# Optimization experiments

Hardware: AMD Instinct MI355X
Metric: run time of the kernel (lower is better)

Reference implementation:

```python
import jax, jax.numpy as jnp
import numpy as np

EMB = 1024
HEADS = 8
EXP = 4
EPS = 1e-5


def setup_inputs() -> dict:
    key = jax.random.key(0)
    ks = jax.random.split(key, 12)
    s = 0.02
    return {
        "x": jax.random.normal(ks[0], (4, 2048, EMB), dtype=jnp.float32),
        "wqkv_w": jax.random.normal(ks[1], (EMB, 3 * EMB), dtype=jnp.float32) * s,
        "wqkv_b": jnp.zeros((3 * EMB,), dtype=jnp.float32),
        "proj_w": jax.random.normal(ks[2], (EMB, EMB), dtype=jnp.float32) * s,
        "proj_b": jnp.zeros((EMB,), dtype=jnp.float32),
        "lin1_w": jax.random.normal(ks[3], (EMB, EXP * EMB), dtype=jnp.float32) * s,
        "lin1_b": jnp.zeros((EXP * EMB,), dtype=jnp.float32),
        "lin2_w": jax.random.normal(ks[4], (EXP * EMB, EMB), dtype=jnp.float32) * s,
        "lin2_b": jnp.zeros((EMB,), dtype=jnp.float32),
        "ln_g": jnp.ones((EMB,), dtype=jnp.float32),
        "ln_b": jnp.zeros((EMB,), dtype=jnp.float32),
    }


def _layernorm(x, g, b):
    mu = jnp.mean(x, axis=-1, keepdims=True)
    var = jnp.var(x, axis=-1, keepdims=True)
    return (x - mu) * jax.lax.rsqrt(var + EPS) * g + b


def reference(x, wqkv_w, wqkv_b, proj_w, proj_b, lin1_w, lin1_b, lin2_w, lin2_b, ln_g, ln_b):
    b, n, e = x.shape
    h = HEADS
    d = e // h
    # fused QKV; source splits '(h d w)' with w=3 innermost (interleaved)
    w = x @ wqkv_w + wqkv_b                      # [b, n, 3e]
    w = w.reshape(b, n, h, d, 3)
    w = jnp.transpose(w, (4, 0, 2, 1, 3))        # [3, b, h, n, d]
    q, k, v = w[0], w[1], w[2]
    scores = jnp.einsum('bhqd,bhkd->bhqk', q, k)  # unscaled logits (as in source)
    attn = jax.nn.softmax(scores, axis=-1) / jnp.sqrt(jnp.float32(e))
    o = jnp.einsum('bhqk,bhkd->bhqd', attn, v)
    o = jnp.transpose(o, (0, 2, 1, 3)).reshape(b, n, e)
    mha = o @ proj_w + proj_b
    x = _layernorm(x + mha, ln_g, ln_b)
    ff = (jax.nn.gelu(x @ lin1_w + lin1_b, approximate=False)) @ lin2_w + lin2_b
    return _layernorm(x + ff, ln_g, ln_b)
```

## Files before the change

kernel.cpp:

```cpp
#include <hip/hip_runtime.h>
#include <hip/hip_bf16.h>
#include <math.h>

#define B_DIM 4
#define SEQ   2048
#define EMB   1024
#define HEADS 8
#define DHEAD 128
#define M_TOK (B_DIM * SEQ)
#define FFDIM (4 * EMB)

typedef unsigned short u16;
typedef __attribute__((ext_vector_type(8))) short short8v;
typedef __attribute__((ext_vector_type(4))) float float4v;
typedef __attribute__((ext_vector_type(16))) float float16v;

__device__ __forceinline__ u16 f2b(float f) {
  union { float f; unsigned u; } a; a.f = f;
  unsigned u = a.u;
  u += 0x7fffu + ((u >> 16) & 1u);
  return (u16)(u >> 16);
}

__device__ __forceinline__ u16 f2b_hw(float f) {
  __hip_bfloat16 h = __float2bfloat16(f);
  return *(u16*)&h;
}

__device__ __forceinline__ void gload16(const void* g, void* l) {
  __builtin_amdgcn_global_load_lds(
      (const __attribute__((address_space(1))) unsigned int*)g,
      (__attribute__((address_space(3))) unsigned int*)l, 16, 0, 0);
}

__device__ __forceinline__ float gelu_inl(float v) {
  const float y = 0.7978845608028654f * (v + 0.044715f * v * v * v);
  const float e = __expf(2.0f * y);
  const float th = 1.0f - 2.0f / (e + 1.0f);
  return 0.5f * v * (1.0f + th);
}

__device__ __forceinline__ void tcvt_body(const float* __restrict__ W,
    u16* __restrict__ Wt, int K, int N, int bx, int by, int tx, int ty,
    float (*t)[33]) {
  const int n0 = bx * 32, k0 = by * 32;
  for (int j = ty; j < 32; j += 8)
    t[j][tx] = W[(size_t)(k0 + j) * N + n0 + tx];
  __syncthreads();
  for (int j = ty; j < 32; j += 8)
    Wt[(size_t)(n0 + j) * K + k0 + tx] = f2b(t[tx][j]);
}

__global__ __launch_bounds__(256) void k_prep(
    const float* __restrict__ x, const float* __restrict__ wqkv_w,
    const float* __restrict__ proj_w, const float* __restrict__ lin1_w,
    const float* __restrict__ lin2_w, u16* __restrict__ xb,
    u16* __restrict__ wqkv_t, u16* __restrict__ proj_t,
    u16* __restrict__ lin1_t, u16* __restrict__ lin2_t) {
  __shared__ float t[32][33];
  const int bid = blockIdx.x, tid = threadIdx.x;
  if (bid < 8192) {
    const int i = bid * 256 + tid;
    const float4 v = ((const float4*)x)[i];
    unsigned long long pk = (unsigned long long)f2b(v.x)
        | ((unsigned long long)f2b(v.y) << 16)
        | ((unsigned long long)f2b(v.z) << 32)
        | ((unsigned long long)f2b(v.w) << 48);
    ((unsigned long long*)xb)[i] = pk;
    return;
  }
  const int tx = tid & 31, ty = tid >> 5;
  if (bid < 11264)
    tcvt_body(wqkv_w, wqkv_t, 1024, 3072, (bid - 8192) % 96, (bid - 8192) / 96, tx, ty, t);
  else if (bid < 12288)
    tcvt_body(proj_w, proj_t, 1024, 1024, (bid - 11264) % 32, (bid - 11264) / 32, tx, ty, t);
  else if (bid < 16384)
    tcvt_body(lin1_w, lin1_t, 1024, 4096, (bid - 12288) % 128, (bid - 12288) / 128, tx, ty, t);
  else
    tcvt_body(lin2_w, lin2_t, 4096, 1024, (bid - 16384) % 32, (bid - 16384) / 32, tx, ty, t);
}

template <int EPI>
__global__ __launch_bounds__(256, 2) void k_gemm(
    const u16* __restrict__ A, const u16* __restrict__ Bt,
    const float* __restrict__ bias, const float* __restrict__ res,
    void* __restrict__ out0, int M, int N, int K) {
  __shared__ __align__(16) u16 lds[2][2][128][32];
  const int tid = threadIdx.x;
  const int l = tid & 63, w = tid >> 6;
  const int g = l >> 4, lm = l & 15;
  const int wm = w >> 1, wn = w & 1;

  const int NBX = N >> 7;
  const int nwg = NBX * (M >> 7);
  const int wg = blockIdx.x;
  const int swz = (wg & 7) * (nwg >> 3) + (wg >> 3);
  const int tn = swz % NBX, tm = swz / NBX;

  const size_t arow0 = (size_t)tm * 128;
  const size_t brow0 = (size_t)tn * 128;
  const int srow = l >> 2;
  const int scol = (l & 3) * 8;

  float4v acc[4][4];
  const float4v vzero = {0.f, 0.f, 0.f, 0.f};
#pragma unroll
  for (int i = 0; i < 4; ++i)
#pragma unroll
    for (int j = 0; j < 4; ++j) acc[i][j] = vzero;

  const int nt = K / 32;
  auto stage = [&](int t, int buf) {
    const int k0 = t * 32;
#pragma unroll
    for (int i = 0; i < 2; ++i) {
      const int r = w * 32 + i * 16 + srow;
      gload16(A + (arow0 + r) * (size_t)K + k0 + scol, &lds[buf][0][w * 32 + i * 16][0]);
      gload16(Bt + (brow0 + r) * (size_t)K + k0 + scol, &lds[buf][1][w * 32 + i * 16][0]);
    }
  };

  stage(0, 0);
  __syncthreads();
  for (int t = 0; t < nt; ++t) {
    const int buf = t & 1;
    if (t + 1 < nt) stage(t + 1, buf ^ 1);
    short8v af[4], bf[4];
#pragma unroll
    for (int mf = 0; mf < 4; ++mf)
      af[mf] = *(const short8v*)&lds[buf][0][wm * 64 + mf * 16 + lm][g * 8];
#pragma unroll
    for (int nf = 0; nf < 4; ++nf)
      bf[nf] = *(const short8v*)&lds[buf][1][wn * 64 + nf * 16 + lm][g * 8];
#pragma unroll
    for (int mf = 0; mf < 4; ++mf)
#pragma unroll
      for (int nf = 0; nf < 4; ++nf)
        acc[mf][nf] = __builtin_amdgcn_mfma_f32_16x16x32_bf16(af[mf], bf[nf], acc[mf][nf], 0, 0, 0);
    __syncthreads();
  }

#pragma unroll
  for (int mf = 0; mf < 4; ++mf)
#pragma unroll
    for (int nf = 0; nf < 4; ++nf)
#pragma unroll
      for (int r = 0; r < 4; ++r) {
        const int row = tm * 128 + wm * 64 + mf * 16 + 4 * g + r;
        const int col = tn * 128 + wn * 64 + nf * 16 + lm;
        float v = acc[mf][nf][r] + bias[col];
        if constexpr (EPI == 0) {
          const int hh = col / 384;
          const int rem = col - hh * 384;
          const int d = rem / 3;
          const int wv = rem - d * 3;
          const int btok = row >> 11, ntok = row & 2047;
          u16* dst = (u16*)out0 + (size_t)wv * ((size_t)M_TOK * EMB)
                   + (((size_t)(btok * HEADS + hh) * SEQ + ntok) * DHEAD + d);
          *dst = f2b(v);
        } else if constexpr (EPI == 2) {
          ((u16*)out0)[(size_t)row * N + col] = f2b(gelu_inl(v));
        } else {
          const size_t idx = (size_t)row * N + col;
          ((float*)out0)[idx] = v + res[idx];
        }
      }
}

__global__ __launch_bounds__(512, 2) void k_attn(
    const u16* __restrict__ q, const u16* __restrict__ k,
    const u16* __restrict__ v, u16* __restrict__ o) {
  __shared__ __align__(16) u16 KT[128 * 128];
  __shared__ __align__(16) u16 VT[128 * 128];
  const int tid = threadIdx.x;
  const int l = tid & 63, w = tid >> 6;
  const int q32 = l & 31, hi = l >> 5;
  const int qt = blockIdx.x, hh = blockIdx.y, bb = blockIdx.z;
  const size_t base = (size_t)(bb * HEADS + hh) * SEQ * DHEAD;
  const int qrow0 = qt * 256 + w * 32;

  short8v qf[8];
#pragma unroll
  for (int c = 0; c < 8; ++c)
    qf[c] = *(const short8v*)(q + base + (size_t)(qrow0 + q32) * DHEAD + c * 16 + hi * 8);

  float m = -1e30f, Sden = 0.f;
  float16v O[4];
#pragma unroll
  for (int nf = 0; nf < 4; ++nf)
#pragma unroll
    for (int r = 0; r < 16; ++r) O[nf][r] = 0.f;

  const int krow = tid >> 4;
  const int kseg = (tid & 15) * 16;
  const int vp = tid & 31, vdg = tid >> 5;

  for (int kvt = 0; kvt < 16; ++kvt) {
    const size_t kvbase = base + (size_t)kvt * 128 * DHEAD;
#pragma unroll
    for (int s = 0; s < 4; ++s) {
      const int r = s * 32 + krow;
      const int csrc = kseg ^ ((r & 7) << 4);
      gload16(k + kvbase + r * DHEAD + (csrc >> 1), (u16*)KT + s * 4096 + tid * 8);
    }
#pragma unroll
    for (int kk = 0; kk < 2; ++kk) {
      const int d0 = vdg * 8;
      const u16* s0p = v + kvbase + (size_t)(kk * 64 + 2 * vp) * DHEAD + d0;
      const short8v a = *(const short8v*)s0p;
      const short8v b2 = *(const short8v*)(s0p + DHEAD);
#pragma unroll
      for (int j = 0; j < 8; ++j) {
        const unsigned pk = ((unsigned)(u16)a[j]) | (((unsigned)(u16)b2[j]) << 16);
        const int byte = ((d0 + j) * 256 + kk * 128 + 4 * vp) ^ (((d0 + j) & 7) << 4);
        *(unsigned*)((char*)VT + byte) = pk;
      }
    }
    __syncthreads();

#pragma unroll
    for (int sub = 0; sub < 2; ++sub) {
      float16v S0, S1;
#pragma unroll
      for (int r = 0; r < 16; ++r) { S0[r] = 0.f; S1[r] = 0.f; }
      __builtin_amdgcn_s_setprio(1);
#pragma unroll
      for (int c = 0; c < 8; ++c) {
        const int cb = (c * 32 + hi * 16) ^ ((q32 & 7) << 4);
        const short8v kf0 = *(const short8v*)((const char*)KT + (sub * 64 + q32) * 256 + cb);
        const short8v kf1 = *(const short8v*)((const char*)KT + (sub * 64 + 32 + q32) * 256 + cb);
        S0 = __builtin_amdgcn_mfma_f32_32x32x16_bf16(kf0, qf[c], S0, 0, 0, 0);
        S1 = __builtin_amdgcn_mfma_f32_32x32x16_bf16(kf1, qf[c], S1, 0, 0, 0);
      }
      __builtin_amdgcn_s_setprio(0);

      float pm = -1e30f;
#pragma unroll
      for (int r = 0; r < 16; ++r) pm = fmaxf(pm, fmaxf(S0[r], S1[r]));
      pm = fmaxf(pm, __shfl_xor(pm, 32));
      if (!__all(pm <= m + 8.0f)) {
        const float nm = fmaxf(m, pm);
        const float rsc = __expf(m - nm);
        m = nm;
        Sden *= rsc;
#pragma unroll
        for (int r = 0; r < 16; ++r) {
          const float rr_ = __shfl(rsc, (r & 3) + 8 * (r >> 2) + 4 * hi, 64);
#pragma unroll
          for (int nf = 0; nf < 4; ++nf) O[nf][r] *= rr_;
        }
      }
      float ps = 0.f;
#pragma unroll
      for (int r = 0; r < 16; ++r) { S0[r] = __expf(S0[r] - m); ps += S0[r]; }
#pragma unroll
      for (int r = 0; r < 16; ++r) { S1[r] = __expf(S1[r] - m); ps += S1[r]; }
      ps += __shfl_xor(ps, 32);
      Sden += ps;

      unsigned u0[8], u1[8];
#pragma unroll
      for (int j = 0; j < 8; ++j) {
        u0[j] = (unsigned)f2b_hw(S0[2 * j]) | ((unsigned)f2b_hw(S0[2 * j + 1]) << 16);
        u1[j] = (unsigned)f2b_hw(S1[2 * j]) | ((unsigned)f2b_hw(S1[2 * j + 1]) << 16);
      }

#pragma unroll
      for (int ks = 0; ks < 4; ++ks) {
        const int k1 = ks & 1;
        unsigned b0v, b1v, b2v, b3v;
        if (ks < 2) { b0v = u0[4 * k1]; b1v = u0[4 * k1 + 1]; b2v = u0[4 * k1 + 2]; b3v = u0[4 * k1 + 3]; }
        else        { b0v = u1[4 * k1]; b1v = u1[4 * k1 + 1]; b2v = u1[4 * k1 + 2]; b3v = u1[4 * k1 + 3]; }
        const unsigned send0 = hi ? b0v : b2v;
        const unsigned send1 = hi ? b1v : b3v;
        const unsigned rx0 = (unsigned)__shfl_xor((int)send0, 32);
        const unsigned rx1 = (unsigned)__shfl_xor((int)send1, 32);
        union { unsigned uu[4]; short8v s8; } pu;
        pu.uu[0] = hi ? rx0 : b0v;
        pu.uu[1] = hi ? rx1 : b1v;
        pu.uu[2] = hi ? b2v : rx0;
        pu.uu[3] = hi ? b3v : rx1;
        __builtin_amdgcn_s_setprio(1);
#pragma unroll
        for (int nf = 0; nf < 4; ++nf) {
          const int dr = nf * 32 + q32;
          const int vb = (dr * 256 + sub * 128 + ks * 32 + hi * 16) ^ ((dr & 7) << 4);
          const short8v vf = *(const short8v*)((const char*)VT + vb);
          O[nf] = __builtin_amdgcn_mfma_f32_32x32x16_bf16(pu.s8, vf, O[nf], 0, 0, 0);
        }
        __builtin_amdgcn_s_setprio(0);
      }
    }
    __syncthreads();
  }

  const float si = 1.0f / (Sden * 32.0f);
#pragma unroll
  for (int r = 0; r < 16; ++r) {
    const int cr = (r & 3) + 8 * (r >> 2) + 4 * hi;
    const float sio = __shfl(si, cr, 64);
    const int tok = qrow0 + cr;
#pragma unroll
    for (int nf = 0; nf < 4; ++nf)
      o[(size_t)(bb * SEQ + tok) * EMB + hh * DHEAD + nf * 32 + q32] = f2b_hw(O[nf][r] * sio);
  }
}

template <int MODE>
__global__ __launch_bounds__(256) void k_ln(const float* __restrict__ in,
    const float* __restrict__ gw, const float* __restrict__ bw,
    float* __restrict__ outf, u16* __restrict__ outb) {
  __shared__ float ps[4], pq[4];
  const int row = blockIdx.x;
  const int t = threadIdx.x;
  const float4 v = ((const float4*)(in + (size_t)row * EMB))[t];
  float s = v.x + v.y + v.z + v.w;
  float sq = v.x * v.x + v.y * v.y + v.z * v.z + v.w * v.w;
#pragma unroll
  for (int d = 1; d < 64; d <<= 1) { s += __shfl_xor(s, d); sq += __shfl_xor(sq, d); }
  const int l = t & 63, w = t >> 6;
  if (l == 0) { ps[w] = s; pq[w] = sq; }
  __syncthreads();
  s = ps[0] + ps[1] + ps[2] + ps[3];
  sq = pq[0] + pq[1] + pq[2] + pq[3];
  const float mean = s * (1.0f / 1024.0f);
  const float var = sq * (1.0f / 1024.0f) - mean * mean;
  const float rs = rsqrtf(var + 1e-5f);
  const float4 gv = ((const float4*)gw)[t];
  const float4 bv = ((const float4*)bw)[t];
  float4 ov;
  ov.x = (v.x - mean) * rs * gv.x + bv.x;
  ov.y = (v.y - mean) * rs * gv.y + bv.y;
  ov.z = (v.z - mean) * rs * gv.z + bv.z;
  ov.w = (v.w - mean) * rs * gv.w + bv.w;
  ((float4*)(outf + (size_t)row * EMB))[t] = ov;
  if constexpr (MODE == 0) {
    unsigned long long pk = (unsigned long long)f2b(ov.x)
        | ((unsigned long long)f2b(ov.y) << 16)
        | ((unsigned long long)f2b(ov.z) << 32)
        | ((unsigned long long)f2b(ov.w) << 48);
    ((unsigned long long*)(outb + (size_t)row * EMB))[t] = pk;
  }
}

extern "C" void kernel_launch(void* const* d_in, const int* in_sizes, int n_in,
                              void* d_out, int out_size, void* d_ws, size_t ws_size,
                              hipStream_t stream) {
  const float* x      = (const float*)d_in[0];
  const float* wqkv_w = (const float*)d_in[1];
  const float* wqkv_b = (const float*)d_in[2];
  const float* proj_w = (const float*)d_in[3];
  const float* proj_b = (const float*)d_in[4];
  const float* lin1_w = (const float*)d_in[5];
  const float* lin1_b = (const float*)d_in[6];
  const float* lin2_w = (const float*)d_in[7];
  const float* lin2_b = (const float*)d_in[8];
  const float* ln_g   = (const float*)d_in[9];
  const float* ln_b   = (const float*)d_in[10];

  char* ws = (char*)d_ws;
  u16*   wqkv_t = (u16*)(ws + 0);
  u16*   proj_t = (u16*)(ws + 6291456);
  u16*   lin1_t = (u16*)(ws + 8388608);
  u16*   lin2_t = (u16*)(ws + 16777216);
  u16*   qbuf   = (u16*)(ws + 25165824);
  u16*   kbuf   = (u16*)(ws + 25165824 + 16777216);
  u16*   vbuf   = (u16*)(ws + 25165824 + 33554432);
  u16*   xb     = (u16*)(ws + 75497472);
  u16*   attn_o = (u16*)(ws + 75497472);
  float* res1   = (float*)(ws + 92274688);
  u16*   hbuf   = (u16*)(ws + 92274688);
  float* x1f    = (float*)(ws + 25165824);
  u16*   x1b    = (u16*)(ws + 58720256);
  float* outf   = (float*)d_out;

  k_prep<<<20480, 256, 0, stream>>>(x, wqkv_w, proj_w, lin1_w, lin2_w,
                                    xb, wqkv_t, proj_t, lin1_t, lin2_t);

  k_gemm<0><<<(3 * EMB / 128) * (M_TOK / 128), 256, 0, stream>>>(
      xb, wqkv_t, wqkv_b, nullptr, (void*)qbuf, M_TOK, 3 * EMB, EMB);
  k_attn<<<dim3(SEQ / 256, HEADS, B_DIM), 512, 0, stream>>>(qbuf, kbuf, vbuf, attn_o);
  k_gemm<1><<<(EMB / 128) * (M_TOK / 128), 256, 0, stream>>>(
      attn_o, proj_t, proj_b, x, (void*)res1, M_TOK, EMB, EMB);
  k_ln<0><<<M_TOK, 256, 0, stream>>>(res1, ln_g, ln_b, x1f, x1b);
  k_gemm<2><<<(FFDIM / 128) * (M_TOK / 128), 256, 0, stream>>>(
      x1b, lin1_t, lin1_b, nullptr, (void*)hbuf, M_TOK, FFDIM, EMB);
  k_gemm<3><<<(EMB / 128) * (M_TOK / 128), 256, 0, stream>>>(
      hbuf, lin2_t, lin2_b, x1f, (void*)outf, M_TOK, EMB, FFDIM);
  k_ln<1><<<M_TOK, 256, 0, stream>>>(outf, ln_g, ln_b, outf, nullptr);
}
```

Before: 455.7 us.

## Double-buffer attention K/V tiles and remap blocks so each XCD shares heads

```diff
diff --git a/kernel.cpp b/kernel.cpp
--- a/kernel.cpp
+++ b/kernel.cpp
@@ -170,12 +170,16 @@
 __global__ __launch_bounds__(512, 2) void k_attn(
     const u16* __restrict__ q, const u16* __restrict__ k,
     const u16* __restrict__ v, u16* __restrict__ o) {
-  __shared__ __align__(16) u16 KT[128 * 128];
-  __shared__ __align__(16) u16 VT[128 * 128];
+  __shared__ __align__(16) u16 KT[2][64 * 128];
+  __shared__ __align__(16) u16 VT[2][64 * 128];
   const int tid = threadIdx.x;
   const int l = tid & 63, w = tid >> 6;
   const int q32 = l & 31, hi = l >> 5;
-  const int qt = blockIdx.x, hh = blockIdx.y, bb = blockIdx.z;
+  const int i = blockIdx.x;
+  const int xcd = i & 7, j = i >> 3;
+  const int bh = xcd * 4 + (j >> 3);
+  const int qt = j & 7;
+  const int hh = bh & 7, bb = bh >> 3;
   const size_t base = (size_t)(bb * HEADS + hh) * SEQ * DHEAD;
   const int qrow0 = qt * 256 + w * 32;
 
@@ -195,102 +199,115 @@
   const int kseg = (tid & 15) * 16;
   const int vp = tid & 31, vdg = tid >> 5;
 
-  for (int kvt = 0; kvt < 16; ++kvt) {
-    const size_t kvbase = base + (size_t)kvt * 128 * DHEAD;
-#pragma unroll
-    for (int s = 0; s < 4; ++s) {
+  short8v va, vb2;
+  auto loadV = [&](int t) {
+    const u16* s0p = v + base + ((size_t)t * 64 + 2 * vp) * DHEAD + vdg * 8;
+    va  = *(const short8v*)s0p;
+    vb2 = *(const short8v*)(s0p + DHEAD);
+  };
+  auto writeV = [&](int b) {
+    const int d0 = vdg * 8;
+#pragma unroll
+    for (int jj = 0; jj < 8; ++jj) {
+      const unsigned pk = ((unsigned)(u16)va[jj]) | (((unsigned)(u16)vb2[jj]) << 16);
+      const int byte = ((d0 + jj) * 128 + 4 * vp) ^ (((d0 + jj) & 7) << 4);
+      *(unsigned*)((char*)&VT[b][0] + byte) = pk;
+    }
+  };
+  auto stageK = [&](int t, int b) {
+    const size_t kvbase = base + (size_t)t * 64 * DHEAD;
+#pragma unroll
+    for (int s = 0; s < 2; ++s) {
       const int r = s * 32 + krow;
       const int csrc = kseg ^ ((r & 7) << 4);
-      gload16(k + kvbase + r * DHEAD + (csrc >> 1), (u16*)KT + s * 4096 + tid * 8);
-    }
-#pragma unroll
-    for (int kk = 0; kk < 2; ++kk) {
-      const int d0 = vdg * 8;
-      const u16* s0p = v + kvbase + (size_t)(kk * 64 + 2 * vp) * DHEAD + d0;
-      const short8v a = *(const short8v*)s0p;
-      const short8v b2 = *(const short8v*)(s0p + DHEAD);
-#pragma unroll
-      for (int j = 0; j < 8; ++j) {
-        const unsigned pk = ((unsigned)(u16)a[j]) | (((unsigned)(u16)b2[j]) << 16);
-        const int byte = ((d0 + j) * 256 + kk * 128 + 4 * vp) ^ (((d0 + j) & 7) << 4);
-        *(unsigned*)((char*)VT + byte) = pk;
+      gload16(k + kvbase + (size_t)r * DHEAD + (csrc >> 1),
+              (u16*)&KT[b][0] + s * 4096 + tid * 8);
+    }
+  };
+
+  loadV(0);
+  stageK(0, 0);
+  writeV(0);
+  __syncthreads();
+
+  for (int t = 0; t < 32; ++t) {
+    const int buf = t & 1;
+    const char* KTb = (const char*)&KT[buf][0];
+    const char* VTb = (const char*)&VT[buf][0];
+    if (t + 1 < 32) { loadV(t + 1); stageK(t + 1, buf ^ 1); }
+
+    float16v S0, S1;
+#pragma unroll
+    for (int r = 0; r < 16; ++r) { S0[r] = 0.f; S1[r] = 0.f; }
+    __builtin_amdgcn_s_setprio(1);
+#pragma unroll
+    for (int c = 0; c < 8; ++c) {
+      const int cb = (c * 32 + hi * 16) ^ ((q32 & 7) << 4);
+      const short8v kf0 = *(const short8v*)(KTb + q32 * 256 + cb);
+      const short8v kf1 = *(const short8v*)(KTb + (32 + q32) * 256 + cb);
+      S0 = __builtin_amdgcn_mfma_f32_32x32x16_bf16(kf0, qf[c], S0, 0, 0, 0);
+      S1 = __builtin_amdgcn_mfma_f32_32x32x16_bf16(kf1, qf[c], S1, 0, 0, 0);
+    }
+    __builtin_amdgcn_s_setprio(0);
+
+    float pm = -1e30f;
+#pragma unroll
+    for (int r = 0; r < 16; ++r) pm = fmaxf(pm, fmaxf(S0[r], S1[r]));
+    pm = fmaxf(pm, __shfl_xor(pm, 32));
+    if (!__all(pm <= m + 8.0f)) {
+      const float nm = fmaxf(m, pm);
+      const float rsc = __expf(m - nm);
+      m = nm;
+      Sden *= rsc;
+#pragma unroll
+      for (int r = 0; r < 16; ++r) {
+        const float rr_ = __shfl(rsc, (r & 3) + 8 * (r >> 2) + 4 * hi, 64);
+#pragma unroll
+        for (int nf = 0; nf < 4; ++nf) O[nf][r] *= rr_;
       }
     }
-    __syncthreads();
-
-#pragma unroll
-    for (int sub = 0; sub < 2; ++sub) {
-      float16v S0, S1;
-#pragma unroll
-      for (int r = 0; r < 16; ++r) { S0[r] = 0.f; S1[r] = 0.f; }
+    float ps = 0.f;
+#pragma unroll
+    for (int r = 0; r < 16; ++r) { S0[r] = __expf(S0[r] - m); ps += S0[r]; }
+#pragma unroll
+    for (int r = 0; r < 16; ++r) { S1[r] = __expf(S1[r] - m); ps += S1[r]; }
+    ps += __shfl_xor(ps, 32);
+    Sden += ps;
+
+    unsigned u0[8], u1[8];
+#pragma unroll
+    for (int jj = 0; jj < 8; ++jj) {
+      u0[jj] = (unsigned)f2b_hw(S0[2 * jj]) | ((unsigned)f2b_hw(S0[2 * jj + 1]) << 16);
+      u1[jj] = (unsigned)f2b_hw(S1[2 * jj]) | ((unsigned)f2b_hw(S1[2 * jj + 1]) << 16);
+    }
+
+#pragma unroll
+    for (int ks = 0; ks < 4; ++ks) {
+      const int k1 = ks & 1;
+      unsigned b0v, b1v, b2v, b3v;
+      if (ks < 2) { b0v = u0[4 * k1]; b1v = u0[4 * k1 + 1]; b2v = u0[4 * k1 + 2]; b3v = u0[4 * k1 + 3]; }
+      else        { b0v = u1[4 * k1]; b1v = u1[4 * k1 + 1]; b2v = u1[4 * k1 + 2]; b3v = u1[4 * k1 + 3]; }
+      const unsigned send0 = hi ? b0v : b2v;
+      const unsigned send1 = hi ? b1v : b3v;
+      const unsigned rx0 = (unsigned)__shfl_xor((int)send0, 32);
+      const unsigned rx1 = (unsigned)__shfl_xor((int)send1, 32);
+      union { unsigned uu[4]; short8v s8; } pu;
+      pu.uu[0] = hi ? rx0 : b0v;
+      pu.uu[1] = hi ? rx1 : b1v;
+      pu.uu[2] = hi ? b2v : rx0;
+      pu.uu[3] = hi ? b3v : rx1;
       __builtin_amdgcn_s_setprio(1);
 #pragma unroll
-      for (int c = 0; c < 8; ++c) {
-        const int cb = (c * 32 + hi * 16) ^ ((q32 & 7) << 4);
-        const short8v kf0 = *(const short8v*)((const char*)KT + (sub * 64 + q32) * 256 + cb);
-        const short8v kf1 = *(const short8v*)((const char*)KT + (sub * 64 + 32 + q32) * 256 + cb);
-        S0 = __builtin_amdgcn_mfma_f32_32x32x16_bf16(kf0, qf[c], S0, 0, 0, 0);
-        S1 = __builtin_amdgcn_mfma_f32_32x32x16_bf16(kf1, qf[c], S1, 0, 0, 0);
+      for (int nf = 0; nf < 4; ++nf) {
+        const int dr = nf * 32 + q32;
+        const int vb = (dr * 128 + ks * 32 + hi * 16) ^ ((dr & 7) << 4);
+        const short8v vf = *(const short8v*)(VTb + vb);
+        O[nf] = __builtin_amdgcn_mfma_f32_32x32x16_bf16(pu.s8, vf, O[nf], 0, 0, 0);
       }
       __builtin_amdgcn_s_setprio(0);
-
-      float pm = -1e30f;
-#pragma unroll
-      for (int r = 0; r < 16; ++r) pm = fmaxf(pm, fmaxf(S0[r], S1[r]));
-      pm = fmaxf(pm, __shfl_xor(pm, 32));
-      if (!__all(pm <= m + 8.0f)) {
-        const float nm = fmaxf(m, pm);
-        const float rsc = __expf(m - nm);
-        m = nm;
-        Sden *= rsc;
-#pragma unroll
-        for (int r = 0; r < 16; ++r) {
-          const float rr_ = __shfl(rsc, (r & 3) + 8 * (r >> 2) + 4 * hi, 64);
-#pragma unroll
-          for (int nf = 0; nf < 4; ++nf) O[nf][r] *= rr_;
-        }
-      }
-      float ps = 0.f;
-#pragma unroll
-      for (int r = 0; r < 16; ++r) { S0[r] = __expf(S0[r] - m); ps += S0[r]; }
-#pragma unroll
-      for (int r = 0; r < 16; ++r) { S1[r] = __expf(S1[r] - m); ps += S1[r]; }
-      ps += __shfl_xor(ps, 32);
-      Sden += ps;
-
-      unsigned u0[8], u1[8];
-#pragma unroll
-      for (int j = 0; j < 8; ++j) {
-        u0[j] = (unsigned)f2b_hw(S0[2 * j]) | ((unsigned)f2b_hw(S0[2 * j + 1]) << 16);
-        u1[j] = (unsigned)f2b_hw(S1[2 * j]) | ((unsigned)f2b_hw(S1[2 * j + 1]) << 16);
-      }
-
-#pragma unroll
-      for (int ks = 0; ks < 4; ++ks) {
-        const int k1 = ks & 1;
-        unsigned b0v, b1v, b2v, b3v;
-        if (ks < 2) { b0v = u0[4 * k1]; b1v = u0[4 * k1 + 1]; b2v = u0[4 * k1 + 2]; b3v = u0[4 * k1 + 3]; }
-        else        { b0v = u1[4 * k1]; b1v = u1[4 * k1 + 1]; b2v = u1[4 * k1 + 2]; b3v = u1[4 * k1 + 3]; }
-        const unsigned send0 = hi ? b0v : b2v;
-        const unsigned send1 = hi ? b1v : b3v;
-        const unsigned rx0 = (unsigned)__shfl_xor((int)send0, 32);
-        const unsigned rx1 = (unsigned)__shfl_xor((int)send1, 32);
-        union { unsigned uu[4]; short8v s8; } pu;
-        pu.uu[0] = hi ? rx0 : b0v;
-        pu.uu[1] = hi ? rx1 : b1v;
-        pu.uu[2] = hi ? b2v : rx0;
-        pu.uu[3] = hi ? b3v : rx1;
-        __builtin_amdgcn_s_setprio(1);
-#pragma unroll
-        for (int nf = 0; nf < 4; ++nf) {
-          const int dr = nf * 32 + q32;
-          const int vb = (dr * 256 + sub * 128 + ks * 32 + hi * 16) ^ ((dr & 7) << 4);
-          const short8v vf = *(const short8v*)((const char*)VT + vb);
-          O[nf] = __builtin_amdgcn_mfma_f32_32x32x16_bf16(pu.s8, vf, O[nf], 0, 0, 0);
-        }
-        __builtin_amdgcn_s_setprio(0);
-      }
-    }
+    }
+
+    if (t + 1 < 32) writeV(buf ^ 1);
     __syncthreads();
   }
 
@@ -379,7 +396,7 @@
 
   k_gemm<0><<<(3 * EMB / 128) * (M_TOK / 128), 256, 0, stream>>>(
       xb, wqkv_t, wqkv_b, nullptr, (void*)qbuf, M_TOK, 3 * EMB, EMB);
-  k_attn<<<dim3(SEQ / 256, HEADS, B_DIM), 512, 0, stream>>>(qbuf, kbuf, vbuf, attn_o);
+  k_attn<<<256, 512, 0, stream>>>(qbuf, kbuf, vbuf, attn_o);
   k_gemm<1><<<(EMB / 128) * (M_TOK / 128), 256, 0, stream>>>(
       attn_o, proj_t, proj_b, x, (void*)res1, M_TOK, EMB, EMB);
   k_ln<0><<<M_TOK, 256, 0, stream>>>(res1, ln_g, ln_b, x1f, x1b);
```

New measurement: 455.1 us. No clear change (-0.1%).
